# Optimization experiments

Hardware: AMD Instinct MI355X
Metric: run time of the kernel (lower is better)

The kernel has to match this reference:

```python
import jax, jax.numpy as jnp
import numpy as np

L = 20        # num layers (TTS LM)
Q = 512       # query length
PAST = 512    # past_kv_len
END = PAST + Q  # end_step = 1024
MAXS = 2048   # max_seq_len
D = 896       # hidden size
NKV = 2       # KV heads
NQ = 14       # Q heads
G = NQ // NKV # GQA repeat = 7
HD = 64       # head dim
FF = 4864     # SwiGLU intermediate (Qwen2.5-0.5B)
EPS = 1e-6
SCALE = 1.0 / np.sqrt(HD)


def rms_norm(x, w):
    return x * jax.lax.rsqrt(jnp.mean(x * x, axis=-1, keepdims=True) + EPS) * w


def rotate_half(x):
    x1, x2 = jnp.split(x, 2, axis=-1)
    return jnp.concatenate([-x2, x1], axis=-1)


def setup_inputs() -> dict:
    key = jax.random.key(0)
    ks = jax.random.split(key, 24)
    s = 0.02
    inp = {
        'hidden_states': jax.random.normal(ks[0], (1, Q, D), jnp.float32),
        'position_cos': jax.random.uniform(ks[1], (1, Q, HD), jnp.float32, -1.0, 1.0),
        'position_sin': jax.random.uniform(ks[2], (1, Q, HD), jnp.float32, -1.0, 1.0),
        'attention_mask': jnp.zeros((1, 1, Q, END), jnp.float32),
        'inject_mode': jnp.zeros((1,), jnp.float32),
        'inject_k': jax.random.normal(ks[3], (1, L * NKV, Q, HD), jnp.float32),
        'inject_v': jax.random.normal(ks[4], (1, L * NKV, Q, HD), jnp.float32),
        'k_cache': (jax.random.normal(ks[5], (L, 1, NKV, MAXS, HD), jnp.float32) * 0.5).astype(jnp.float16),
        'v_cache': (jax.random.normal(ks[6], (L, 1, NKV, MAXS, HD), jnp.float32) * 0.5).astype(jnp.float16),
        'Wq': jax.random.normal(ks[7], (L, D, NQ * HD), jnp.float32) * s,
        'bq': jax.random.normal(ks[8], (L, NQ * HD), jnp.float32) * s,
        'Wk': jax.random.normal(ks[9], (L, D, NKV * HD), jnp.float32) * s,
        'bk': jax.random.normal(ks[10], (L, NKV * HD), jnp.float32) * s,
        'Wv': jax.random.normal(ks[11], (L, D, NKV * HD), jnp.float32) * s,
        'bv': jax.random.normal(ks[12], (L, NKV * HD), jnp.float32) * s,
        'Wo': jax.random.normal(ks[13], (L, NQ * HD, D), jnp.float32) * s,
        'ln1': jnp.ones((L, D), jnp.float32),
        'ln2': jnp.ones((L, D), jnp.float32),
        'Wg': jax.random.normal(ks[14], (L, D, FF), jnp.float32) * s,
        'Wu': jax.random.normal(ks[15], (L, D, FF), jnp.float32) * s,
        'Wd': jax.random.normal(ks[16], (L, FF, D), jnp.float32) * s,
        'final_w': jnp.ones((D,), jnp.float32),
    }
    return inp


def reference(hidden_states, position_cos, position_sin, attention_mask,
              inject_mode, inject_k, inject_v, k_cache, v_cache,
              Wq, bq, Wk, bk, Wv, bv, Wo, ln1, ln2, Wg, Wu, Wd, final_w):
    cos = position_cos[:, None]   # [1,1,Q,HD]
    sin = position_sin[:, None]
    inj = inject_mode[0]
    normal = 1.0 - inj
    mask = attention_mask[:, None]  # [1,1,1,Q,END] broadcast over (g,h)
    # per-layer inject slices: [L,1,NKV,Q,HD]
    ik = jnp.transpose(inject_k.reshape(1, L, NKV, Q, HD), (1, 0, 2, 3, 4))
    iv = jnp.transpose(inject_v.reshape(1, L, NKV, Q, HD), (1, 0, 2, 3, 4))

    def layer_fn(h, p):
        (wq, bq_, wk, bk_, wv, bv_, wo, l1, l2, wg, wu, wd, kc, vc, ikl, ivl) = p
        residual = h
        x = rms_norm(h, l1)
        q = (x @ wq + bq_).reshape(1, Q, NQ, HD).transpose(0, 2, 1, 3)   # [1,NQ,Q,HD]
        k = (x @ wk + bk_).reshape(1, Q, NKV, HD).transpose(0, 2, 1, 3)  # [1,NKV,Q,HD]
        v = (x @ wv + bv_).reshape(1, Q, NKV, HD).transpose(0, 2, 1, 3)
        q = q * cos + rotate_half(q) * sin
        k = k * cos + rotate_half(k) * sin
        k = normal * k + inj * ikl
        v = normal * v + inj * ivl
        kc = kc.at[:, :, PAST:END].set(k.astype(jnp.float16))
        vc = vc.at[:, :, PAST:END].set(v.astype(jnp.float16))
        kf = kc[:, :, :END].astype(jnp.float32)  # [1,NKV,END,HD]
        vf = vc[:, :, :END].astype(jnp.float32)
        qg = q.reshape(1, NKV, G, Q, HD)         # grouped GQA (== repeat_kv)
        scores = jnp.einsum('bghqd,bgkd->bghqk', qg, kf) * SCALE + mask
        w = jax.nn.softmax(scores, axis=-1)
        o = jnp.einsum('bghqk,bgkd->bghqd', w, vf)
        o = o.reshape(1, NQ, Q, HD).transpose(0, 2, 1, 3).reshape(1, Q, NQ * HD)
        h = residual + o @ wo
        residual = h
        x = rms_norm(h, l2)
        h = residual + (jax.nn.silu(x @ wg) * (x @ wu)) @ wd
        return h, None

    xs = (Wq, bq, Wk, bk, Wv, bv, Wo, ln1, ln2, Wg, Wu, Wd, k_cache, v_cache, ik, iv)
    h, _ = jax.lax.scan(layer_fn, hidden_states, xs)
    return rms_norm(h, final_w)
```

## Files before the change

### kernel.cpp

```cpp
#include <hip/hip_runtime.h>
#include <hip/hip_fp16.h>
#include <hip/hip_cooperative_groups.h>

namespace cg = cooperative_groups;

#define NLAYER 20
#define QLEN 512
#define PAST 512
#define ENDS 1024
#define MAXS 2048
#define DMODEL 896
#define NKV 2
#define NQ 14
#define GQ 7
#define HD 64
#define FF 4864
#define RMSEPS 1e-6f
#define ATT_SCALE 0.125f

typedef _Float16 f16x8 __attribute__((ext_vector_type(8)));
typedef float f32x4 __attribute__((ext_vector_type(4)));
typedef unsigned int u32_;

__device__ __forceinline__ void gld16(const void* g, void* l) {
    __builtin_amdgcn_global_load_lds(
        (const __attribute__((address_space(1))) u32_*)g,
        (__attribute__((address_space(3))) u32_*)l, 16, 0, 0);
}

union SmemU {
    struct { __half As[8192]; __half Bs[8192]; } g;
    struct { __half S[16512]; float rowinv[16]; } a;
    struct { float T[32][33]; } p;
    struct { float red[4]; } r;
};

__device__ __forceinline__ void gemm_body(
    const __half* __restrict__ A, int lda, const __half* __restrict__ B, int ldb,
    float* __restrict__ outP, __half* __restrict__ actP, int N, int Kps, int mode,
    int bx, int by, int bz, int t, __half* As, __half* Bs)
{
    const int lane = t & 63, wave = t >> 6;
    const int wm = wave >> 1, wn = wave & 1;
    const int m0 = by * 128, n0 = bx * 128;
    const int kb0 = bz * Kps;
    const int sr = t >> 2, sc = (t & 3) * 8;
    const int la = lane & 15, ka = (lane >> 4) * 8;
    const int nIter = Kps >> 5;
    const size_t a0 = (size_t)(m0 + sr) * lda + kb0 + sc;
    const size_t a1 = (size_t)(m0 + sr + 64) * lda + kb0 + sc;
    const size_t b0 = (size_t)(n0 + sr) * ldb + kb0 + sc;
    const size_t b1 = (size_t)(n0 + sr + 64) * ldb + kb0 + sc;
    const int l0 = sr * 32 + sc, l1 = (sr + 64) * 32 + sc;

    f32x4 acc[4][4] = {};
    gld16(&A[a0], &As[l0]);
    gld16(&A[a1], &As[l1]);
    gld16(&B[b0], &Bs[l0]);
    gld16(&B[b1], &Bs[l1]);
    int buf = 0;
    for (int kt = 0; kt < nIter; kt++) {
        __syncthreads();
        if (kt + 1 < nIter) {
            const int ko = (kt + 1) * 32;
            gld16(&A[a0 + ko], &As[(buf ^ 1) * 4096 + l0]);
            gld16(&A[a1 + ko], &As[(buf ^ 1) * 4096 + l1]);
            gld16(&B[b0 + ko], &Bs[(buf ^ 1) * 4096 + l0]);
            gld16(&B[b1 + ko], &Bs[(buf ^ 1) * 4096 + l1]);
        }
        f16x8 av[4], bv[4];
#pragma unroll
        for (int i = 0; i < 4; i++) av[i] = *(const f16x8*)&As[buf * 4096 + (wm * 64 + i * 16 + la) * 32 + ka];
#pragma unroll
        for (int j = 0; j < 4; j++) bv[j] = *(const f16x8*)&Bs[buf * 4096 + (wn * 64 + j * 16 + la) * 32 + ka];
#pragma unroll
        for (int i = 0; i < 4; i++)
#pragma unroll
            for (int j = 0; j < 4; j++)
                acc[i][j] = __builtin_amdgcn_mfma_f32_16x16x32_f16(av[i], bv[j], acc[i][j], 0, 0, 0);
        buf ^= 1;
    }
    __syncthreads();
    const int r0 = m0 + wm * 64 + (lane >> 4) * 4;
    const int c0 = n0 + wn * 64 + la;
    if (mode == 0) {
        float* o = outP + (size_t)bz * QLEN * N;
#pragma unroll
        for (int i = 0; i < 4; i++)
#pragma unroll
            for (int j = 0; j < 4; j++)
#pragma unroll
                for (int r = 0; r < 4; r++)
                    o[(size_t)(r0 + i * 16 + r) * N + c0 + j * 16] = acc[i][j][r];
    } else {
#pragma unroll
        for (int i = 0; i < 4; i++)
#pragma unroll
            for (int j = 0; j < 4; j++)
#pragma unroll
                for (int r = 0; r < 4; r++) {
                    float v = acc[i][j][r];
                    float other = __shfl_xor(v, 1);
                    if (!(la & 1)) {
                        const int c = c0 + j * 16;
                        const int row = r0 + i * 16 + r;
                        float sg = v / (1.f + __expf(-v));
                        actP[(size_t)row * FF + (c >> 1)] = __float2half(sg * other);
                    }
                }
    }
}

__device__ __forceinline__ void prep_body(
    const float* __restrict__ Wq, const float* __restrict__ Wk, const float* __restrict__ Wv,
    const float* __restrict__ Wo, const float* __restrict__ Wg, const float* __restrict__ Wu,
    const float* __restrict__ Wd, int layer, int z, int bx, int t, float (*T)[33],
    __half* __restrict__ dstW)
{
    const int K = (z == 3) ? FF : DMODEL;
    const int N = (z == 0) ? 1152 : (z == 2) ? 2 * FF : DMODEL;
    const int tilesN = N / 32;
    const int tk = bx / tilesN, tn = bx % tilesN;
    const int k0 = tk * 32, n0 = tn * 32;
    const float* src; int ldn, nc0; int isU = 0;
    if (z == 0) {
        if (n0 < 896)       { src = Wq + (size_t)layer * 896 * 896; ldn = 896; nc0 = n0; }
        else if (n0 < 1024) { src = Wk + (size_t)layer * 896 * 128; ldn = 128; nc0 = n0 - 896; }
        else                { src = Wv + (size_t)layer * 896 * 128; ldn = 128; nc0 = n0 - 1024; }
    } else if (z == 1) { src = Wo + (size_t)layer * 896 * 896; ldn = 896; nc0 = n0; }
    else if (z == 2) {
        if (n0 < FF) { src = Wg + (size_t)layer * 896 * FF; ldn = FF; nc0 = n0; }
        else         { src = Wu + (size_t)layer * 896 * FF; ldn = FF; nc0 = n0 - FF; isU = 1; }
    } else { src = Wd + (size_t)layer * FF * 896; ldn = 896; nc0 = n0; }

    const int r = t >> 3, c4 = (t & 7) * 4;
    float4 v = *(const float4*)&src[(size_t)(k0 + r) * ldn + nc0 + c4];
    T[r][c4 + 0] = v.x; T[r][c4 + 1] = v.y; T[r][c4 + 2] = v.z; T[r][c4 + 3] = v.w;
    __syncthreads();
    const int drow = (z == 2) ? (2 * (nc0 + r) + isU) : (n0 + r);
    __half* dst = dstW + (size_t)drow * K + k0 + c4;
    __half2 p0 = __halves2half2(__float2half_rn(T[c4 + 0][r]), __float2half_rn(T[c4 + 1][r]));
    __half2 p1 = __halves2half2(__float2half_rn(T[c4 + 2][r]), __float2half_rn(T[c4 + 3][r]));
    *(__half2*)dst = p0;
    *(__half2*)(dst + 2) = p1;
    __syncthreads();
}

__device__ __forceinline__ void prep_dispatch(
    const float* Wq, const float* Wk, const float* Wv, const float* Wo,
    const float* Wg, const float* Wu, const float* Wd,
    const float* bq, const float* bk, const float* bv,
    int layer, int j, int t, float (*T)[33],
    __half* wq, __half* wo, __half* wgu, __half* wd, float* bqkv)
{
    int z; __half* dst; int bx = j;
    if (j < 1008)       { z = 0; dst = wq; }
    else if (j < 1792)  { z = 1; dst = wo;  bx -= 1008; }
    else if (j < 10304) { z = 2; dst = wgu; bx -= 1792; }
    else                { z = 3; dst = wd;  bx -= 10304; }
    prep_body(Wq, Wk, Wv, Wo, Wg, Wu, Wd, layer, z, bx, t, T, dst);
    if (z == 0 && bx == 0) {
        for (int i = t; i < 1152; i += 256) {
            float b = (i < 896) ? bq[(size_t)layer * 896 + i]
                    : (i < 1024) ? bk[(size_t)layer * 128 + i - 896]
                                 : bv[(size_t)layer * 128 + i - 1024];
            bqkv[i] = b;
        }
    }
}

__device__ __forceinline__ void ropekv_body(
    const float* __restrict__ part, const float* __restrict__ bias,
    const float* __restrict__ cosb, const float* __restrict__ sinb,
    const float* __restrict__ injm, const float* __restrict__ injk,
    const float* __restrict__ injv, const float* __restrict__ kc32,
    const float* __restrict__ vc32, int layer, int nsplit,
    __half* __restrict__ qr, __half* __restrict__ Ka, __half* __restrict__ Vt,
    int p, int lt)
{
    const int kvh = lt >> 6, d = lt & 63;
    if (p < PAST) {
        const size_t idx = (((size_t)layer * NKV + kvh) * MAXS + p) * HD + d;
        Ka[((size_t)kvh * ENDS + p) * HD + d] = __float2half(kc32[idx]);
        Vt[((size_t)kvh * HD + d) * ENDS + p] = __float2half(vc32[idx]);
        return;
    }
    const int pn = p - PAST;
    const float inj = injm[0], nrm = 1.f - inj;
    const float* rb = part + (size_t)pn * 1152;
    const size_t sst = (size_t)QLEN * 1152;
    auto rsum = [&](int c) {
        float x = bias[c];
        for (int s = 0; s < nsplit; s++) x += rb[(size_t)s * sst + c];
        return x;
    };
    for (int idx = lt; idx < NQ * HD; idx += 128) {
        const int dd = idx & 63;
        float x = rsum(idx);
        int pc = (dd < 32) ? idx + 32 : idx - 32;
        float pv = rsum(pc);
        if (dd < 32) pv = -pv;
        float rv = x * cosb[pn * HD + dd] + pv * sinb[pn * HD + dd];
        qr[((size_t)(idx >> 6) * QLEN + pn) * HD + dd] = __float2half(rv);
    }
    {
        const int c = NQ * HD + lt;
        float x = rsum(c);
        int pc = (d < 32) ? c + 32 : c - 32;
        float pv = rsum(pc);
        if (d < 32) pv = -pv;
        float rv = x * cosb[pn * HD + d] + pv * sinb[pn * HD + d];
        float kn = nrm * rv + inj * injk[(((size_t)layer * NKV + kvh) * QLEN + pn) * HD + d];
        Ka[((size_t)kvh * ENDS + PAST + pn) * HD + d] = __float2half(kn);
        const int cv = NQ * HD + NKV * HD + lt;
        float vv = rsum(cv);
        float vn = nrm * vv + inj * injv[(((size_t)layer * NKV + kvh) * QLEN + pn) * HD + d];
        Vt[((size_t)kvh * HD + d) * ENDS + PAST + pn] = __float2half(vn);
    }
}

__device__ __forceinline__ int sswz(int row, int col) {
    return row * 1032 + (col ^ ((row & 7) << 3));
}

__device__ __forceinline__ void attn_body(
    const __half* __restrict__ qr, const __half* __restrict__ Ka,
    const __half* __restrict__ Vt, const float* __restrict__ mask,
    __half* __restrict__ ob, int q0, int h, int t, __half* S, float* rowinv)
{
    const int kv = h / GQ;
    const int lane = t & 63, w = t >> 6;
    const int la = lane & 15, kg = lane >> 4;

    const f16x8* qp = (const f16x8*)&qr[((size_t)h * QLEN + q0 + la) * HD + kg * 8];
    const f16x8 qa0 = qp[0], qa1 = qp[4];

    for (int kb = 0; kb < 256; kb += 16) {
        const int key = w * 256 + kb + la;
        const f16x8* kp = (const f16x8*)&Ka[((size_t)kv * ENDS + key) * HD + kg * 8];
        f32x4 s4 = {0.f, 0.f, 0.f, 0.f};
        s4 = __builtin_amdgcn_mfma_f32_16x16x32_f16(qa0, kp[0], s4, 0, 0, 0);
        s4 = __builtin_amdgcn_mfma_f32_16x16x32_f16(qa1, kp[4], s4, 0, 0, 0);
#pragma unroll
        for (int r = 0; r < 4; r++) {
            const int row = kg * 4 + r;
            float sv = s4[r] * ATT_SCALE + mask[(size_t)(q0 + row) * ENDS + key];
            S[sswz(row, key)] = __float2half(sv);
        }
    }
    __syncthreads();
    {
        const int row = w * 4 + kg;
        float mx = -1e30f;
        for (int j = 0; j < 64; j++)
            mx = fmaxf(mx, __half2float(S[sswz(row, la + 16 * j)]));
        for (int o = 1; o < 16; o <<= 1) mx = fmaxf(mx, __shfl_xor(mx, o));
        float sum = 0.f;
        for (int j = 0; j < 64; j++) {
            const int idx = sswz(row, la + 16 * j);
            float e = __expf(__half2float(S[idx]) - mx);
            S[idx] = __float2half(e);
            sum += e;
        }
        for (int o = 1; o < 16; o <<= 1) sum += __shfl_xor(sum, o);
        if (la == 0) rowinv[row] = 1.f / sum;
    }
    __syncthreads();
    {
        const int d = 16 * w + la;
        const __half* vrow = &Vt[((size_t)kv * HD + d) * ENDS];
        f32x4 acc = {0.f, 0.f, 0.f, 0.f};
        for (int ks = 0; ks < ENDS; ks += 32) {
            f16x8 pa = *(const f16x8*)&S[sswz(la, ks + kg * 8)];
            f16x8 vb = *(const f16x8*)&vrow[ks + kg * 8];
            acc = __builtin_amdgcn_mfma_f32_16x16x32_f16(pa, vb, acc, 0, 0, 0);
        }
#pragma unroll
        for (int r = 0; r < 4; r++) {
            const int qrow = kg * 4 + r;
            ob[(size_t)(q0 + qrow) * (NQ * HD) + h * HD + d] =
                __float2half(acc[r] * rowinv[qrow]);
        }
    }
    __syncthreads();
}

__device__ inline void cvt_store(float* p, float v)  { *p = v; }
__device__ inline void cvt_store(__half* p, float v) { *p = __float2half(v); }

template <typename OUT>
__device__ __forceinline__ void rms_body(
    float* __restrict__ h, const float* __restrict__ parts, int nparts,
    const float* __restrict__ w, OUT* __restrict__ out, int m, int t,
    float* red, float scale)
{
    float loc[4];
    float ss = 0.f;
    int r = 0;
    for (int i = t; i < DMODEL; i += 256, r++) {
        float x = h[(size_t)m * DMODEL + i];
        for (int s = 0; s < nparts; s++)
            x += parts[(size_t)s * QLEN * DMODEL + (size_t)m * DMODEL + i];
        loc[r] = x;
        if (nparts) h[(size_t)m * DMODEL + i] = x;
        ss += x * x;
    }
    for (int o = 32; o; o >>= 1) ss += __shfl_xor(ss, o);
    if ((t & 63) == 0) red[t >> 6] = ss;
    __syncthreads();
    float rs = rsqrtf((red[0] + red[1] + red[2] + red[3]) / (float)DMODEL + RMSEPS);
    r = 0;
    for (int i = t; i < DMODEL; i += 256, r++)
        cvt_store(&out[(size_t)m * DMODEL + i], loc[r] * rs * w[i] * scale);
    __syncthreads();
}

struct P22 {
    const float *hidden, *cosb, *sinb, *mask, *injm, *injk, *injv, *kc32, *vc32;
    const float *Wq, *bq, *Wk, *bk, *Wv, *bv, *Wo, *ln1, *ln2, *Wg, *Wu, *Wd, *finw;
    float *h; __half *xn, *qr, *Ka, *Vt, *ob, *act; float *BIGR;
    float *bqkv0, *bqkv1;
    __half *wq0, *wo0, *wgu0, *wd0, *wq1, *wo1, *wgu1, *wd1;
    float *outF;
};

__global__ __launch_bounds__(256) void mega_kernel(P22 P)
{
    __shared__ SmemU sm;
    cg::grid_group gg = cg::this_grid();
    const int nb = gridDim.x, bid = blockIdx.x, t = threadIdx.x;

    for (int j = bid; j < 1792; j += nb) {
        int i = j * 256 + t;
        if (i < QLEN * DMODEL) P.h[i] = P.hidden[i];
    }
    for (int j = bid; j < 14560; j += nb)
        prep_dispatch(P.Wq, P.Wk, P.Wv, P.Wo, P.Wg, P.Wu, P.Wd, P.bq, P.bk, P.bv,
                      0, j, t, sm.p.T, P.wq0, P.wo0, P.wgu0, P.wd0, P.bqkv0);
    gg.sync();

    for (int l = 0; l < NLAYER; l++) {
        const int pb = l & 1;
        const __half* wq  = pb ? P.wq1  : P.wq0;
        const __half* wo  = pb ? P.wo1  : P.wo0;
        const __half* wgu = pb ? P.wgu1 : P.wgu0;
        const __half* wd  = pb ? P.wd1  : P.wd0;
        const float*  bqk = pb ? P.bqkv1 : P.bqkv0;

        for (int j = bid; j < QLEN; j += nb)
            rms_body<__half>(P.h, l ? P.BIGR : nullptr, l ? 8 : 0,
                             P.ln1 + (size_t)l * DMODEL, P.xn, j, t, sm.r.red, 1.f);
        gg.sync();

        for (int j = bid; j < 252; j += nb) {
            int z = j / 36, r = j % 36;
            gemm_body(P.xn, DMODEL, wq, DMODEL, P.BIGR, nullptr, 1152, 128, 0,
                      r % 9, r / 9, z, t, sm.g.As, sm.g.Bs);
        }
        gg.sync();

        for (int j = bid; j < 512; j += nb)
            ropekv_body(P.BIGR, bqk, P.cosb, P.sinb, P.injm, P.injk, P.injv,
                        P.kc32, P.vc32, l, 7, P.qr, P.Ka, P.Vt,
                        j * 2 + (t >> 7), t & 127);
        gg.sync();

        for (int j = bid; j < 448; j += nb)
            attn_body(P.qr, P.Ka, P.Vt, P.mask, P.ob, (j & 31) * 16, j >> 5, t,
                      sm.a.S, sm.a.rowinv);
        gg.sync();

        for (int j = bid; j < 196; j += nb) {
            int z = j / 28, r = j % 28;
            gemm_body(P.ob, DMODEL, wo, DMODEL, P.BIGR, nullptr, DMODEL, 128, 0,
                      r % 7, r / 7, z, t, sm.g.As, sm.g.Bs);
        }
        gg.sync();

        for (int j = bid; j < QLEN; j += nb)
            rms_body<__half>(P.h, P.BIGR, 7, P.ln2 + (size_t)l * DMODEL, P.xn,
                             j, t, sm.r.red, 1.f);
        gg.sync();

        {
            const int extra = (l + 1 < NLAYER) ? 14560 : 0;
            const int npb = (l + 1) & 1;
            __half* nwq  = npb ? P.wq1  : P.wq0;
            __half* nwo  = npb ? P.wo1  : P.wo0;
            __half* nwgu = npb ? P.wgu1 : P.wgu0;
            __half* nwd  = npb ? P.wd1  : P.wd0;
            float*  nbq  = npb ? P.bqkv1 : P.bqkv0;
            for (int j = bid; j < 304 + extra; j += nb) {
                if (j < 304)
                    gemm_body(P.xn, DMODEL, wgu, DMODEL, nullptr, P.act, 2 * FF, DMODEL, 1,
                              j % 76, j / 76, 0, t, sm.g.As, sm.g.Bs);
                else
                    prep_dispatch(P.Wq, P.Wk, P.Wv, P.Wo, P.Wg, P.Wu, P.Wd, P.bq, P.bk, P.bv,
                                  l + 1, j - 304, t, sm.p.T, nwq, nwo, nwgu, nwd, nbq);
            }
        }
        gg.sync();

        for (int j = bid; j < 224; j += nb) {
            int z = j / 28, r = j % 28;
            gemm_body(P.act, FF, wd, FF, P.BIGR, nullptr, DMODEL, 608, 0,
                      r % 7, r / 7, z, t, sm.g.As, sm.g.Bs);
        }
        gg.sync();
    }
    for (int j = bid; j < QLEN; j += nb)
        rms_body<float>(P.h, P.BIGR, 8, P.finw, P.outF, j, t, sm.r.red, 1.f);
}

__global__ __launch_bounds__(256) void init_kernel(
    const float* __restrict__ hidden, float* __restrict__ h, int* __restrict__ flags)
{
    const int idx = blockIdx.x * 256 + threadIdx.x;
    if (blockIdx.x == 0 && threadIdx.x < 8) flags[threadIdx.x] = 0;
    if (idx < QLEN * DMODEL) h[idx] = hidden[idx];
}

__global__ __launch_bounds__(256) void prep_all(
    const float* Wq, const float* Wk, const float* Wv, const float* Wo,
    const float* Wg, const float* Wu, const float* Wd,
    const float* bq, const float* bk, const float* bv, int layer,
    __half* wqkv, __half* wo, __half* wgu, __half* wd, float* bqkv)
{
    __shared__ float T[32][33];
    prep_dispatch(Wq, Wk, Wv, Wo, Wg, Wu, Wd, bq, bk, bv, layer, blockIdx.x,
                  threadIdx.x, T, wqkv, wo, wgu, wd, bqkv);
}

__global__ __launch_bounds__(256) void gemm128(
    const __half* A, int lda, const __half* B, int ldb,
    float* outP, __half* actP, int N, int Kps, int mode)
{
    __shared__ SmemU sm;
    gemm_body(A, lda, B, ldb, outP, actP, N, Kps, mode,
              blockIdx.x, blockIdx.y, blockIdx.z, threadIdx.x, sm.g.As, sm.g.Bs);
}

__global__ __launch_bounds__(128) void ropekv_kernel(
    const float* part, const float* bias, const float* cosb, const float* sinb,
    const float* injm, const float* injk, const float* injv,
    const float* kc32, const float* vc32, int layer, int nsplit,
    __half* qr, __half* Ka, __half* Vt)
{
    ropekv_body(part, bias, cosb, sinb, injm, injk, injv, kc32, vc32,
                layer, nsplit, qr, Ka, Vt, blockIdx.x, threadIdx.x);
}

__global__ __launch_bounds__(256) void attn_mfma(
    const __half* qr, const __half* Ka, const __half* Vt, const float* mask, __half* ob)
{
    __shared__ SmemU sm;
    attn_body(qr, Ka, Vt, mask, ob, blockIdx.x * 16, blockIdx.y, threadIdx.x,
              sm.a.S, sm.a.rowinv);
}

template <typename OUT>
__global__ __launch_bounds__(256) void rms_kernel(
    float* h, const float* parts, int nparts, const float* w, OUT* out,
    const int* flags)
{
    __shared__ float red[4];
    float scale = 1.f;
    if (flags) {
        int E = flags[1] + 2 * flags[3] + 4 * flags[5];
        for (int i = 0; i < E; i++) scale *= 3.f;
    }
    rms_body<OUT>(h, parts, nparts, w, out, blockIdx.x, threadIdx.x, red, scale);
}

__global__ __launch_bounds__(256) void check_gemm(
    const __half* A, int lda, const __half* B, int K,
    const float* part, int N, int nz, int* flags)
{
    const int t = threadIdx.x;
    const int m = (t >> 4) * 33;
    const int n = ((t & 15) * 997) % N;
    float acc = 0.f;
    for (int k = 0; k < K; k++)
        acc += __half2float(A[(size_t)m * lda + k]) * __half2float(B[(size_t)n * K + k]);
    float got = 0.f;
    for (int z = 0; z < nz; z++) got += part[(size_t)z * QLEN * N + (size_t)m * N + n];
    if (fabsf(acc - got) > 0.03f) atomicOr(&flags[1], 1);
}

extern "C" void kernel_launch(void* const* d_in, const int* in_sizes, int n_in,
                              void* d_out, int out_size, void* d_ws, size_t ws_size,
                              hipStream_t stream)
{
    const float*  hidden = (const float*)d_in[0];
    const float*  cosb   = (const float*)d_in[1];
    const float*  sinb   = (const float*)d_in[2];
    const float*  mask   = (const float*)d_in[3];
    const float*  injm   = (const float*)d_in[4];
    const float*  injk   = (const float*)d_in[5];
    const float*  injv   = (const float*)d_in[6];
    const float*  kc32   = (const float*)d_in[7];
    const float*  vc32   = (const float*)d_in[8];
    const float*  Wq     = (const float*)d_in[9];
    const float*  bq     = (const float*)d_in[10];
    const float*  Wk     = (const float*)d_in[11];
    const float*  bk     = (const float*)d_in[12];
    const float*  Wv     = (const float*)d_in[13];
    const float*  bv     = (const float*)d_in[14];
    const float*  Wo     = (const float*)d_in[15];
    const float*  ln1    = (const float*)d_in[16];
    const float*  ln2    = (const float*)d_in[17];
    const float*  Wg     = (const float*)d_in[18];
    const float*  Wu     = (const float*)d_in[19];
    const float*  Wd     = (const float*)d_in[20];
    const float*  finw   = (const float*)d_in[21];

    bool size_ok = (n_in == 22) &&
        in_sizes[0] == 458752 && in_sizes[1] == 32768 && in_sizes[3] == 524288 &&
        in_sizes[4] == 1 && in_sizes[5] == 1310720 && in_sizes[7] == 5242880 &&
        in_sizes[9] == 16056320 && in_sizes[10] == 17920 && in_sizes[11] == 2293760 &&
        in_sizes[15] == 16056320 && in_sizes[16] == 17920 && in_sizes[18] == 87162880 &&
        in_sizes[20] == 87162880 && in_sizes[21] == 896;
    if (!size_ok) { hipMemsetAsync(d_out, 0x42, (size_t)out_size * 4, stream); return; }

    char* ws = (char*)d_ws;
    size_t off = 0;
    auto alloc = [&](size_t bytes) { void* p = ws + off; off += (bytes + 255) & ~255ull; return p; };
    int*    flags = (int*)alloc(256);
    float*  bqkv0 = (float*)alloc(1152 * 4);
    float*  bqkv1 = (float*)alloc(1152 * 4);
    float*  h     = (float*)alloc((size_t)QLEN * DMODEL * 4);
    __half* xn    = (__half*)alloc((size_t)QLEN * DMODEL * 2);
    __half* qr    = (__half*)alloc((size_t)NQ * QLEN * HD * 2);
    __half* Ka    = (__half*)alloc((size_t)NKV * ENDS * HD * 2);
    __half* Vt    = (__half*)alloc((size_t)NKV * ENDS * HD * 2);
    __half* ob    = (__half*)alloc((size_t)QLEN * NQ * HD * 2);
    __half* act   = (__half*)alloc((size_t)QLEN * FF * 2);
    float*  BIGR  = (float*)alloc(7ull * QLEN * 1152 * 4);
    __half* wq0   = (__half*)alloc(2064384);
    __half* wo0   = (__half*)alloc(1605632);
    __half* wgu0  = (__half*)alloc(17432576);
    __half* wd0   = (__half*)alloc(8716288);
    const size_t NEED_LEGACY = off;
    __half* wq1   = (__half*)alloc(2064384);
    __half* wo1   = (__half*)alloc(1605632);
    __half* wgu1  = (__half*)alloc(17432576);
    __half* wd1   = (__half*)alloc(8716288);
    const size_t NEED_MEGA = off;

    if (ws_size < NEED_LEGACY) {
        hipMemsetAsync(d_out, 0, (size_t)out_size * 4, stream);
        return;
    }

    bool mega_ok = (ws_size >= NEED_MEGA);
    if (mega_ok) {
        int maxB = 0;
        hipError_t e = hipOccupancyMaxActiveBlocksPerMultiprocessor(
            &maxB, reinterpret_cast<const void*>(&mega_kernel), 256, 0);
        if (e != hipSuccess || maxB < 1) mega_ok = false;
        if (mega_ok) {
            int grid = maxB * 256;
            if (grid > 1024) grid = 1024;
            P22 Pv = { hidden, cosb, sinb, mask, injm, injk, injv, kc32, vc32,
                       Wq, bq, Wk, bk, Wv, bv, Wo, ln1, ln2, Wg, Wu, Wd, finw,
                       h, xn, qr, Ka, Vt, ob, act, BIGR, bqkv0, bqkv1,
                       wq0, wo0, wgu0, wd0, wq1, wo1, wgu1, wd1, (float*)d_out };
            void* args[] = { (void*)&Pv };
            hipError_t le = hipLaunchCooperativeKernel(
                reinterpret_cast<const void*>(&mega_kernel),
                dim3(grid), dim3(256), args, 0, stream);
            if (le == hipSuccess) return;
            mega_ok = false;
        }
    }

    init_kernel<<<1792, 256, 0, stream>>>(hidden, h, flags);
    for (int l = 0; l < NLAYER; l++) {
        prep_all<<<14560, 256, 0, stream>>>(Wq, Wk, Wv, Wo, Wg, Wu, Wd, bq, bk, bv, l,
                                            wq0, wo0, wgu0, wd0, bqkv0);
        rms_kernel<__half><<<QLEN, 256, 0, stream>>>(h, l ? BIGR : nullptr, l ? 8 : 0,
                                                     ln1 + (size_t)l * DMODEL, xn, nullptr);
        gemm128<<<dim3(9, 4, 7), 256, 0, stream>>>(xn, DMODEL, wq0, DMODEL, BIGR, nullptr, 1152, 128, 0);
        if (l == 0) check_gemm<<<1, 256, 0, stream>>>(xn, DMODEL, wq0, DMODEL, BIGR, 1152, 7, flags);
        ropekv_kernel<<<ENDS, 128, 0, stream>>>(BIGR, bqkv0, cosb, sinb, injm, injk, injv,
                                                kc32, vc32, l, 7, qr, Ka, Vt);
        attn_mfma<<<dim3(32, 14), 256, 0, stream>>>(qr, Ka, Vt, mask, ob);
        gemm128<<<dim3(7, 4, 7), 256, 0, stream>>>(ob, DMODEL, wo0, DMODEL, BIGR, nullptr, DMODEL, 128, 0);
        rms_kernel<__half><<<QLEN, 256, 0, stream>>>(h, BIGR, 7, ln2 + (size_t)l * DMODEL, xn, nullptr);
        gemm128<<<dim3(76, 4, 1), 256, 0, stream>>>(xn, DMODEL, wgu0, DMODEL, nullptr, act, 2 * FF, DMODEL, 1);
        gemm128<<<dim3(7, 4, 8), 256, 0, stream>>>(act, FF, wd0, FF, BIGR, nullptr, DMODEL, 608, 0);
    }
    rms_kernel<float><<<QLEN, 256, 0, stream>>>(h, BIGR, 8, finw, (float*)d_out, flags);
}
```

Before: 3.273 ms.

## Spread next-layer weight prep across all stages, swizzle GEMM LDS, reduce split-K

The next layer's weight conversion and transpose work, previously packed into the gate/up GEMM stage, is now split into chunks and run by otherwise idle blocks in every stage of the cooperative megakernel. This aims to fill idle CUs in the small stages. The GEMM shared-memory layout gets an XOR swizzle on the K columns to cut LDS bank conflicts. Split-K for the QKV and O projections drops from 7 to 4 partitions, which means fewer partial sums to reduce but less parallelism. Extra __syncthreads are added to protect shared-memory reuse between different kinds of work item in the same block.

```diff
diff --git a/kernel.cpp b/kernel.cpp
--- a/kernel.cpp
+++ b/kernel.cpp
@@ -47,10 +47,12 @@
     const int sr = t >> 2, sc = (t & 3) * 8;
     const int la = lane & 15, ka = (lane >> 4) * 8;
     const int nIter = Kps >> 5;
-    const size_t a0 = (size_t)(m0 + sr) * lda + kb0 + sc;
-    const size_t a1 = (size_t)(m0 + sr + 64) * lda + kb0 + sc;
-    const size_t b0 = (size_t)(n0 + sr) * ldb + kb0 + sc;
-    const size_t b1 = (size_t)(n0 + sr + 64) * ldb + kb0 + sc;
+    const int swzS = ((sr >> 1) & 3) << 3;
+    const int scw = sc ^ swzS;
+    const size_t a0 = (size_t)(m0 + sr) * lda + kb0 + scw;
+    const size_t a1 = (size_t)(m0 + sr + 64) * lda + kb0 + scw;
+    const size_t b0 = (size_t)(n0 + sr) * ldb + kb0 + scw;
+    const size_t b1 = (size_t)(n0 + sr + 64) * ldb + kb0 + scw;
     const int l0 = sr * 32 + sc, l1 = (sr + 64) * 32 + sc;
 
     f32x4 acc[4][4] = {};
@@ -70,9 +72,15 @@
         }
         f16x8 av[4], bv[4];
 #pragma unroll
-        for (int i = 0; i < 4; i++) av[i] = *(const f16x8*)&As[buf * 4096 + (wm * 64 + i * 16 + la) * 32 + ka];
-#pragma unroll
-        for (int j = 0; j < 4; j++) bv[j] = *(const f16x8*)&Bs[buf * 4096 + (wn * 64 + j * 16 + la) * 32 + ka];
+        for (int i = 0; i < 4; i++) {
+            const int row = wm * 64 + i * 16 + la;
+            av[i] = *(const f16x8*)&As[buf * 4096 + row * 32 + (ka ^ (((row >> 1) & 3) << 3))];
+        }
+#pragma unroll
+        for (int j = 0; j < 4; j++) {
+            const int row = wn * 64 + j * 16 + la;
+            bv[j] = *(const f16x8*)&Bs[buf * 4096 + row * 32 + (ka ^ (((row >> 1) & 3) << 3))];
+        }
 #pragma unroll
         for (int i = 0; i < 4; i++)
 #pragma unroll
@@ -133,6 +141,7 @@
         else         { src = Wu + (size_t)layer * 896 * FF; ldn = FF; nc0 = n0 - FF; isU = 1; }
     } else { src = Wd + (size_t)layer * FF * 896; ldn = 896; nc0 = n0; }
 
+    __syncthreads();
     const int r = t >> 3, c4 = (t & 7) * 4;
     float4 v = *(const float4*)&src[(size_t)(k0 + r) * ldn + nc0 + c4];
     T[r][c4 + 0] = v.x; T[r][c4 + 1] = v.y; T[r][c4 + 2] = v.z; T[r][c4 + 3] = v.w;
@@ -234,6 +243,7 @@
 
     const f16x8* qp = (const f16x8*)&qr[((size_t)h * QLEN + q0 + la) * HD + kg * 8];
     const f16x8 qa0 = qp[0], qa1 = qp[4];
+    __syncthreads();
 
     for (int kb = 0; kb < 256; kb += 16) {
         const int key = w * 256 + kb + la;
@@ -324,6 +334,23 @@
     float *outF;
 };
 
+#define PC_RMS1 512
+#define PC_QKV  880
+#define PC_ROPE 512
+#define PC_ATTN 2304
+#define PC_O    1824
+#define PC_RMS2 1024
+#define PC_GU   5904
+#define PC_D    1600
+#define PB_RMS1 0
+#define PB_QKV  512
+#define PB_ROPE 1392
+#define PB_ATTN 1904
+#define PB_O    4208
+#define PB_RMS2 6032
+#define PB_GU   7056
+#define PB_D    12960
+
 __global__ __launch_bounds__(256) void mega_kernel(P22 P)
 {
     __shared__ SmemU sm;
@@ -346,67 +373,83 @@
         const __half* wgu = pb ? P.wgu1 : P.wgu0;
         const __half* wd  = pb ? P.wd1  : P.wd0;
         const float*  bqk = pb ? P.bqkv1 : P.bqkv0;
-
-        for (int j = bid; j < QLEN; j += nb)
-            rms_body<__half>(P.h, l ? P.BIGR : nullptr, l ? 8 : 0,
-                             P.ln1 + (size_t)l * DMODEL, P.xn, j, t, sm.r.red, 1.f);
-        gg.sync();
-
-        for (int j = bid; j < 252; j += nb) {
-            int z = j / 36, r = j % 36;
-            gemm_body(P.xn, DMODEL, wq, DMODEL, P.BIGR, nullptr, 1152, 128, 0,
-                      r % 9, r / 9, z, t, sm.g.As, sm.g.Bs);
-        }
-        gg.sync();
-
-        for (int j = bid; j < 512; j += nb)
-            ropekv_body(P.BIGR, bqk, P.cosb, P.sinb, P.injm, P.injk, P.injv,
-                        P.kc32, P.vc32, l, 7, P.qr, P.Ka, P.Vt,
-                        j * 2 + (t >> 7), t & 127);
-        gg.sync();
-
-        for (int j = bid; j < 448; j += nb)
-            attn_body(P.qr, P.Ka, P.Vt, P.mask, P.ob, (j & 31) * 16, j >> 5, t,
-                      sm.a.S, sm.a.rowinv);
-        gg.sync();
-
-        for (int j = bid; j < 196; j += nb) {
-            int z = j / 28, r = j % 28;
-            gemm_body(P.ob, DMODEL, wo, DMODEL, P.BIGR, nullptr, DMODEL, 128, 0,
-                      r % 7, r / 7, z, t, sm.g.As, sm.g.Bs);
-        }
-        gg.sync();
-
-        for (int j = bid; j < QLEN; j += nb)
-            rms_body<__half>(P.h, P.BIGR, 7, P.ln2 + (size_t)l * DMODEL, P.xn,
-                             j, t, sm.r.red, 1.f);
-        gg.sync();
-
-        {
-            const int extra = (l + 1 < NLAYER) ? 14560 : 0;
-            const int npb = (l + 1) & 1;
-            __half* nwq  = npb ? P.wq1  : P.wq0;
-            __half* nwo  = npb ? P.wo1  : P.wo0;
-            __half* nwgu = npb ? P.wgu1 : P.wgu0;
-            __half* nwd  = npb ? P.wd1  : P.wd0;
-            float*  nbq  = npb ? P.bqkv1 : P.bqkv0;
-            for (int j = bid; j < 304 + extra; j += nb) {
-                if (j < 304)
-                    gemm_body(P.xn, DMODEL, wgu, DMODEL, nullptr, P.act, 2 * FF, DMODEL, 1,
-                              j % 76, j / 76, 0, t, sm.g.As, sm.g.Bs);
-                else
-                    prep_dispatch(P.Wq, P.Wk, P.Wv, P.Wo, P.Wg, P.Wu, P.Wd, P.bq, P.bk, P.bv,
-                                  l + 1, j - 304, t, sm.p.T, nwq, nwo, nwgu, nwd, nbq);
-            }
-        }
-        gg.sync();
-
-        for (int j = bid; j < 224; j += nb) {
-            int z = j / 28, r = j % 28;
-            gemm_body(P.act, FF, wd, FF, P.BIGR, nullptr, DMODEL, 608, 0,
-                      r % 7, r / 7, z, t, sm.g.As, sm.g.Bs);
-        }
-        gg.sync();
+        const bool hasN = (l + 1 < NLAYER);
+        __half* nwq  = pb ? P.wq0  : P.wq1;
+        __half* nwo  = pb ? P.wo0  : P.wo1;
+        __half* nwgu = pb ? P.wgu0 : P.wgu1;
+        __half* nwd  = pb ? P.wd0  : P.wd1;
+        float*  nbq  = pb ? P.bqkv0 : P.bqkv1;
+        #define PREPN(idx) prep_dispatch(P.Wq, P.Wk, P.Wv, P.Wo, P.Wg, P.Wu, P.Wd, \
+            P.bq, P.bk, P.bv, l + 1, (idx), t, sm.p.T, nwq, nwo, nwgu, nwd, nbq)
+
+        for (int j = bid; j < QLEN + (hasN ? PC_RMS1 : 0); j += nb) {
+            if (j < QLEN)
+                rms_body<__half>(P.h, l ? P.BIGR : nullptr, l ? 8 : 0,
+                                 P.ln1 + (size_t)l * DMODEL, P.xn, j, t, sm.r.red, 1.f);
+            else PREPN(PB_RMS1 + j - QLEN);
+        }
+        gg.sync();
+
+        for (int j = bid; j < 144 + (hasN ? PC_QKV : 0); j += nb) {
+            if (j < 144) {
+                int z = j / 36, r = j % 36;
+                gemm_body(P.xn, DMODEL, wq, DMODEL, P.BIGR, nullptr, 1152, 224, 0,
+                          r % 9, r / 9, z, t, sm.g.As, sm.g.Bs);
+            } else PREPN(PB_QKV + j - 144);
+        }
+        gg.sync();
+
+        for (int j = bid; j < 512 + (hasN ? PC_ROPE : 0); j += nb) {
+            if (j < 512)
+                ropekv_body(P.BIGR, bqk, P.cosb, P.sinb, P.injm, P.injk, P.injv,
+                            P.kc32, P.vc32, l, 4, P.qr, P.Ka, P.Vt,
+                            j * 2 + (t >> 7), t & 127);
+            else PREPN(PB_ROPE + j - 512);
+        }
+        gg.sync();
+
+        for (int j = bid; j < 448 + (hasN ? PC_ATTN : 0); j += nb) {
+            if (j < 448)
+                attn_body(P.qr, P.Ka, P.Vt, P.mask, P.ob, (j & 31) * 16, j >> 5, t,
+                          sm.a.S, sm.a.rowinv);
+            else PREPN(PB_ATTN + j - 448);
+        }
+        gg.sync();
+
+        for (int j = bid; j < 112 + (hasN ? PC_O : 0); j += nb) {
+            if (j < 112) {
+                int z = j / 28, r = j % 28;
+                gemm_body(P.ob, DMODEL, wo, DMODEL, P.BIGR, nullptr, DMODEL, 224, 0,
+                          r % 7, r / 7, z, t, sm.g.As, sm.g.Bs);
+            } else PREPN(PB_O + j - 112);
+        }
+        gg.sync();
+
+        for (int j = bid; j < QLEN + (hasN ? PC_RMS2 : 0); j += nb) {
+            if (j < QLEN)
+                rms_body<__half>(P.h, P.BIGR, 4, P.ln2 + (size_t)l * DMODEL, P.xn,
+                                 j, t, sm.r.red, 1.f);
+            else PREPN(PB_RMS2 + j - QLEN);
+        }
+        gg.sync();
+
+        for (int j = bid; j < 304 + (hasN ? PC_GU : 0); j += nb) {
+            if (j < 304)
+                gemm_body(P.xn, DMODEL, wgu, DMODEL, nullptr, P.act, 2 * FF, DMODEL, 1,
+                          j % 76, j / 76, 0, t, sm.g.As, sm.g.Bs);
+            else PREPN(PB_GU + j - 304);
+        }
+        gg.sync();
+
+        for (int j = bid; j < 224 + (hasN ? PC_D : 0); j += nb) {
+            if (j < 224) {
+                int z = j / 28, r = j % 28;
+                gemm_body(P.act, FF, wd, FF, P.BIGR, nullptr, DMODEL, 608, 0,
+                          r % 7, r / 7, z, t, sm.g.As, sm.g.Bs);
+            } else PREPN(PB_D + j - 224);
+        }
+        gg.sync();
+        #undef PREPN
     }
     for (int j = bid; j < QLEN; j += nb)
         rms_body<float>(P.h, P.BIGR, 8, P.finw, P.outF, j, t, sm.r.red, 1.f);
@@ -466,7 +509,7 @@
     __shared__ float red[4];
     float scale = 1.f;
     if (flags) {
-        int E = flags[1] + 2 * flags[3] + 4 * flags[5];
+        int E = flags[1];
         for (int i = 0; i < E; i++) scale *= 3.f;
     }
     rms_body<OUT>(h, parts, nparts, w, out, blockIdx.x, threadIdx.x, red, scale);
@@ -535,7 +578,7 @@
     __half* Vt    = (__half*)alloc((size_t)NKV * ENDS * HD * 2);
     __half* ob    = (__half*)alloc((size_t)QLEN * NQ * HD * 2);
     __half* act   = (__half*)alloc((size_t)QLEN * FF * 2);
-    float*  BIGR  = (float*)alloc(7ull * QLEN * 1152 * 4);
+    float*  BIGR  = (float*)alloc(8ull * QLEN * 1152 * 4);
     __half* wq0   = (__half*)alloc(2064384);
     __half* wo0   = (__half*)alloc(1605632);
     __half* wgu0  = (__half*)alloc(17432576);
@@ -580,13 +623,13 @@
                                             wq0, wo0, wgu0, wd0, bqkv0);
         rms_kernel<__half><<<QLEN, 256, 0, stream>>>(h, l ? BIGR : nullptr, l ? 8 : 0,
                                                      ln1 + (size_t)l * DMODEL, xn, nullptr);
-        gemm128<<<dim3(9, 4, 7), 256, 0, stream>>>(xn, DMODEL, wq0, DMODEL, BIGR, nullptr, 1152, 128, 0);
-        if (l == 0) check_gemm<<<1, 256, 0, stream>>>(xn, DMODEL, wq0, DMODEL, BIGR, 1152, 7, flags);
+        gemm128<<<dim3(9, 4, 4), 256, 0, stream>>>(xn, DMODEL, wq0, DMODEL, BIGR, nullptr, 1152, 224, 0);
+        if (l == 0) check_gemm<<<1, 256, 0, stream>>>(xn, DMODEL, wq0, DMODEL, BIGR, 1152, 4, flags);
         ropekv_kernel<<<ENDS, 128, 0, stream>>>(BIGR, bqkv0, cosb, sinb, injm, injk, injv,
-                                                kc32, vc32, l, 7, qr, Ka, Vt);
+                                                kc32, vc32, l, 4, qr, Ka, Vt);
         attn_mfma<<<dim3(32, 14), 256, 0, stream>>>(qr, Ka, Vt, mask, ob);
-        gemm128<<<dim3(7, 4, 7), 256, 0, stream>>>(ob, DMODEL, wo0, DMODEL, BIGR, nullptr, DMODEL, 128, 0);
-        rms_kernel<__half><<<QLEN, 256, 0, stream>>>(h, BIGR, 7, ln2 + (size_t)l * DMODEL, xn, nullptr);
+        gemm128<<<dim3(7, 4, 4), 256, 0, stream>>>(ob, DMODEL, wo0, DMODEL, BIGR, nullptr, DMODEL, 224, 0);
+        rms_kernel<__half><<<QLEN, 256, 0, stream>>>(h, BIGR, 4, ln2 + (size_t)l * DMODEL, xn, nullptr);
         gemm128<<<dim3(76, 4, 1), 256, 0, stream>>>(xn, DMODEL, wgu0, DMODEL, nullptr, act, 2 * FF, DMODEL, 1);
         gemm128<<<dim3(7, 4, 8), 256, 0, stream>>>(act, FF, wd0, FF, BIGR, nullptr, DMODEL, 608, 0);
     }
```

After: 3.005 ms. 8.2% less time.
